# Performance work log

Measured on AMD Instinct MI355X. Metric: run time of the kernel, lower is better.

The kernel has to match this reference:

```python
import jax, jax.numpy as jnp
import numpy as np

N_ENT = 50000
N_REL = 200
DIM = 128
N_BASES = 4
NUM_RELATIONS = 2 * N_REL  # RGCNConv num_relations
E = 200000
S = 20000


def rgcn_conv(x, edge_index, edge_type, edge_norm, basis, att, root, bias, n_nodes):
    """RGCNConv with basis decomposition, aggr='mean'.
    x: [N, Din]; basis: [B, Din, Dout]; att: [R, B]; root: [Din, Dout]; bias: [Dout].
    """
    src, dst = edge_index[0], edge_index[1]
    x_j = x[src]                      # [E, Din] gather
    att_e = att[edge_type]            # [E, B]
    # message: x_j @ (att_e @ basis) without materializing per-edge [Din,Dout] weights
    msg = jnp.einsum('ei,bio,eb->eo', x_j, basis, att_e)  # [E, Dout]
    msg = msg * edge_norm[:, None]
    agg = jax.ops.segment_sum(msg, dst, num_segments=n_nodes)            # [N, Dout]
    cnt = jax.ops.segment_sum(jnp.ones_like(edge_norm), dst, num_segments=n_nodes)
    agg = agg / jnp.maximum(cnt, 1.0)[:, None]            # mean aggregation
    return agg + x @ root + bias


def setup_inputs() -> dict:
    key = jax.random.key(0)
    ks = jax.random.split(key, 20)
    d = {}
    d['entity'] = jnp.arange(N_ENT, dtype=jnp.int64) if jax.config.read('jax_enable_x64') else jnp.arange(N_ENT, dtype=jnp.int32)
    d['edge_index'] = jax.random.randint(ks[0], (2, E), 0, N_ENT)
    d['edge_type'] = jax.random.randint(ks[1], (E,), 0, NUM_RELATIONS)
    d['edge_norm'] = jax.random.uniform(ks[2], (E,), dtype=jnp.float32)
    d['samples'] = jax.random.randint(ks[3], (S, 3), 0, N_REL)
    d['DAD_rel'] = jax.random.normal(ks[4], (N_REL, N_REL), dtype=jnp.float32) * 0.05
    # learned parameters
    d['entity_emb'] = jax.random.normal(ks[5], (N_ENT, DIM), dtype=jnp.float32) * 0.02
    d['relation_emb'] = jax.random.normal(ks[6], (N_REL, DIM), dtype=jnp.float32) * 0.02
    d['entity_context_tab'] = jax.random.normal(ks[7], (N_ENT, DIM), dtype=jnp.float32) * 0.02
    d['relation_context_tab'] = jax.random.normal(ks[8], (N_REL, DIM), dtype=jnp.float32) * 0.02
    d['relation_gcn_weight'] = jax.random.normal(ks[9], (DIM, DIM), dtype=jnp.float32) * 0.02
    d['gate_entity'] = jax.random.uniform(ks[10], (DIM,), dtype=jnp.float32)
    d['gate_relation'] = jax.random.uniform(ks[11], (DIM,), dtype=jnp.float32)
    d['basis1'] = jax.random.normal(ks[12], (N_BASES, DIM, DIM), dtype=jnp.float32) * 0.02
    d['att1'] = jax.random.normal(ks[13], (NUM_RELATIONS, N_BASES), dtype=jnp.float32) * 0.1
    d['root1'] = jax.random.normal(ks[14], (DIM, DIM), dtype=jnp.float32) * 0.02
    d['bias1'] = jnp.zeros((DIM,), dtype=jnp.float32)
    d['basis2'] = jax.random.normal(ks[15], (N_BASES, DIM, DIM), dtype=jnp.float32) * 0.02
    d['att2'] = jax.random.normal(ks[16], (NUM_RELATIONS, N_BASES), dtype=jnp.float32) * 0.1
    d['root2'] = jax.random.normal(ks[17], (DIM, DIM), dtype=jnp.float32) * 0.02
    d['bias2'] = jnp.zeros((DIM,), dtype=jnp.float32)
    return d


def reference(entity, edge_index, edge_type, edge_norm, samples, DAD_rel,
              entity_emb, relation_emb, entity_context_tab, relation_context_tab,
              relation_gcn_weight, gate_entity, gate_relation,
              basis1, att1, root1, bias1, basis2, att2, root2, bias2):
    n_nodes = entity.shape[0]
    ent_ctx = entity_context_tab[entity]                  # [N, D]
    rel_ctx = relation_context_tab                        # arange over all relations -> full table
    ent_ctx = jax.nn.relu(rgcn_conv(ent_ctx, edge_index, edge_type, edge_norm,
                                    basis1, att1, root1, bias1, n_nodes))
    ent_ctx = jax.nn.relu(rgcn_conv(ent_ctx, edge_index, edge_type, edge_norm,
                                    basis2, att2, root2, bias2, n_nodes))
    rel_ctx = jax.nn.relu((DAD_rel @ rel_ctx) @ relation_gcn_weight)
    ge = jax.nn.sigmoid(gate_entity)
    gr = jax.nn.sigmoid(gate_relation)
    h, r, t = samples[:, 0], samples[:, 1], samples[:, 2]
    head_o = ge * entity_emb[h] + (1.0 - ge) * ent_ctx[h]
    rel_o = gr * relation_emb[r] + (1.0 - gr) * rel_ctx[r]
    tail_o = ge * entity_emb[t] + (1.0 - ge) * ent_ctx[t]
    return jnp.stack([head_o, rel_o, tail_o])             # [3, S, D]
```

## Files before the change

### kernel.cpp

```cpp
#include <hip/hip_runtime.h>
#include <hip/hip_bf16.h>

typedef short s8v  __attribute__((ext_vector_type(8)));
typedef float f16v __attribute__((ext_vector_type(16)));

__device__ __forceinline__ unsigned short f2bf(float x) {
    unsigned u = __float_as_uint(x);
    unsigned r = ((u >> 16) & 1u) + 0x7FFFu;
    return (unsigned short)((u + r) >> 16);
}
__device__ __forceinline__ float bf2f(unsigned short h) {
    return __uint_as_float(((unsigned)h) << 16);
}

__global__ __launch_bounds__(256) void prep_kernel(
    const float* __restrict__ basis1, const float* __restrict__ root1,
    const float* __restrict__ basis2, const float* __restrict__ root2,
    unsigned short* __restrict__ Bp1h, unsigned short* __restrict__ Bp2h,
    const int* __restrict__ edge_index, int* __restrict__ deg, int E,
    const float* __restrict__ DAD, const float* __restrict__ rtab,
    const float* __restrict__ Wrel, float* __restrict__ Rc, int NR,
    int b1, int b2)
{
    __shared__ float smem[384];
    const int b = blockIdx.x, tid = threadIdx.x;

    if (b < b1) {
        float* part = smem;
        float* r1s  = smem + 256;
        int r = b;
        int o = tid & 127, q = tid >> 7;
        float s = 0.f;
        for (int j = q; j < NR; j += 2)
            s = fmaf(DAD[r * NR + j], rtab[j * 128 + o], s);
        part[q * 128 + o] = s;
        __syncthreads();
        if (tid < 128) r1s[tid] = part[tid] + part[128 + tid];
        __syncthreads();
        float s2 = 0.f;
        #pragma unroll 8
        for (int k = q * 64; k < q * 64 + 64; ++k)
            s2 = fmaf(r1s[k], Wrel[k * 128 + o], s2);
        part[q * 128 + o] = s2;
        __syncthreads();
        if (tid < 128)
            Rc[r * 128 + tid] = fmaxf(part[tid] + part[128 + tid], 0.f);
    } else if (b < b2) {
        int bb = b - b1;
        int layer = bb >= 320;
        int idx = (layer ? bb - 320 : bb) * 256 + tid;
        int n = idx & 127, k = idx >> 7;
        const float* basis = layer ? basis2 : basis1;
        const float* root  = layer ? root2  : root1;
        float v = (k < 512) ? basis[((k & 3) << 14) + ((k >> 2) << 7) + n]
                            : root[((k - 512) << 7) + n];
        size_t pos = (((size_t)(k >> 3) * 128) + n) * 8 + (k & 7);
        (layer ? Bp2h : Bp1h)[pos] = f2bf(v);
    } else {
        int e = (b - b2) * 256 + tid;
        if (e < E) atomicAdd(&deg[edge_index[E + e]], 1);
    }
}

__global__ __launch_bounds__(1024) void scanA_kernel(
    const int* __restrict__ deg, int* __restrict__ row_start,
    int* __restrict__ btot, int N)
{
    __shared__ int wtot[16];
    __shared__ int woff[16];
    const int tid = threadIdx.x, lane = tid & 63, wid = tid >> 6;
    int i = blockIdx.x * 1024 + tid;
    int v = (i < N) ? deg[i] : 0;
    int x = v;
    #pragma unroll
    for (int d = 1; d < 64; d <<= 1) {
        int t = __shfl_up(x, d, 64);
        if (lane >= d) x += t;
    }
    if (lane == 63) wtot[wid] = x;
    __syncthreads();
    if (wid == 0 && lane < 16) {
        int s = wtot[lane];
        int y = s;
        #pragma unroll
        for (int d = 1; d < 16; d <<= 1) {
            int t = __shfl_up(y, d, 16);
            if (lane >= d) y += t;
        }
        woff[lane] = y - s;
        if (lane == 15) btot[blockIdx.x] = y;
    }
    __syncthreads();
    if (i < N) row_start[i] = woff[wid] + (x - v);
}

__global__ __launch_bounds__(1024) void scanC_kernel(
    int* __restrict__ row_start, int* __restrict__ cursor,
    const int* __restrict__ btot, int nB, int N)
{
    __shared__ int incl[64];
    const int tid = threadIdx.x;
    if (tid < 64) {
        int v = (tid < nB) ? btot[tid] : 0;
        int x = v;
        #pragma unroll
        for (int d = 1; d < 64; d <<= 1) {
            int t = __shfl_up(x, d, 64);
            if (tid >= d) x += t;
        }
        incl[tid] = x;
    }
    __syncthreads();
    int off = (blockIdx.x == 0) ? 0 : incl[blockIdx.x - 1];
    int i = blockIdx.x * 1024 + tid;
    if (i < N) {
        int r = row_start[i] + off;
        row_start[i] = r;
        cursor[i]    = r;
    }
    if (blockIdx.x == (unsigned)(nB - 1) && tid == 0)
        row_start[N] = incl[nB - 1];
}

__global__ __launch_bounds__(256) void fill_kernel(
    const int* __restrict__ edge_index, const int* __restrict__ edge_type,
    const float* __restrict__ edge_norm, int* __restrict__ cursor,
    const float* __restrict__ att1, const float* __restrict__ att2,
    int* __restrict__ src_s, float4* __restrict__ an1, float4* __restrict__ an2, int E,
    const float* __restrict__ tab, const int* __restrict__ entity,
    unsigned short* __restrict__ X0h, unsigned short* __restrict__ X0l, int N,
    int fblocks)
{
    const int b = blockIdx.x, tid = threadIdx.x;
    if (b < fblocks) {
        int e = b * 256 + tid;
        if (e >= E) return;
        int dst = edge_index[E + e];
        int et  = edge_type[e];
        float n = edge_norm[e];
        int pos = atomicAdd(&cursor[dst], 1);
        src_s[pos] = edge_index[e];
        float4 a1 = *(const float4*)&att1[(size_t)et * 4];
        float4 a2 = *(const float4*)&att2[(size_t)et * 4];
        an1[pos] = make_float4(n * a1.x, n * a1.y, n * a1.z, n * a1.w);
        an2[pos] = make_float4(n * a2.x, n * a2.y, n * a2.z, n * a2.w);
    } else {
        int idx = (b - fblocks) * 256 + tid;
        int nn = idx >> 4, part = idx & 15;
        if (nn < N) {
            int src = entity[nn];
            const float4* sp = (const float4*)&tab[(size_t)src * 128 + part * 8];
            float4 v0 = sp[0], v1 = sp[1];
            float vs[8] = {v0.x, v0.y, v0.z, v0.w, v1.x, v1.y, v1.z, v1.w};
            s8v h8, l8;
            #pragma unroll
            for (int j = 0; j < 8; ++j) {
                unsigned short h = f2bf(vs[j]);
                h8[j] = (short)h;
                l8[j] = (short)f2bf(vs[j] - bf2f(h));
            }
            *(s8v*)&X0h[(size_t)nn * 128 + part * 8] = h8;
            *(s8v*)&X0l[(size_t)nn * 128 + part * 8] = l8;
        }
    }
}

__global__ __launch_bounds__(256) void layer_kernel(
    const unsigned short* __restrict__ Xh,
    const unsigned short* __restrict__ Xl,
    const int* __restrict__ row_start,
    const int* __restrict__ src_s,
    const float4* __restrict__ an,
    const unsigned short* __restrict__ Bph,
    const float* __restrict__ bias,
    unsigned short* __restrict__ Xoh,
    unsigned short* __restrict__ Xol,
    int N)
{
    __shared__ unsigned short Whi[64 * 32 * 8];

    const int tid   = threadIdx.x;
    const int node0 = blockIdx.x * 32;

    {
        int g = tid >> 5, l = tid & 31;
        int nb = node0 + g * 4;
        int s0a[4], s1a[4];
        #pragma unroll
        for (int i = 0; i < 4; ++i) {
            int gn = nb + i;
            bool ok = gn < N;
            s0a[i] = ok ? row_start[gn] : 0;
            s1a[i] = ok ? row_start[gn + 1] : 0;
        }
        float acc[4][4][4];
        #pragma unroll
        for (int i = 0; i < 4; ++i)
            #pragma unroll
            for (int d = 0; d < 4; ++d)
                #pragma unroll
                for (int c = 0; c < 4; ++c) acc[i][d][c] = 0.f;

        int need = 0;
        #pragma unroll
        for (int i = 0; i < 4; ++i) need = max(need, s1a[i] - s0a[i]);

        for (int p = 0; p < need; p += 4) {
            #pragma unroll
            for (int i = 0; i < 4; ++i) {
                int q0 = s0a[i] + p;
                if (q0 < s1a[i]) {
                    int se = s1a[i] - 1;
                    int q1 = min(q0 + 1, se);
                    int q2 = min(q0 + 2, se);
                    int q3 = min(q0 + 3, se);
                    int sA = src_s[q0], sB = src_s[q1];
                    int sC = src_s[q2], sD = src_s[q3];
                    float4 aA = an[q0], aB = an[q1];
                    float4 aC = an[q2], aD = an[q3];
                    if (q0 + 1 > se) aB = make_float4(0.f, 0.f, 0.f, 0.f);
                    if (q0 + 2 > se) aC = make_float4(0.f, 0.f, 0.f, 0.f);
                    if (q0 + 3 > se) aD = make_float4(0.f, 0.f, 0.f, 0.f);
                    ushort4 hA = *(const ushort4*)&Xh[(size_t)sA * 128 + (l << 2)];
                    ushort4 hB = *(const ushort4*)&Xh[(size_t)sB * 128 + (l << 2)];
                    ushort4 hC = *(const ushort4*)&Xh[(size_t)sC * 128 + (l << 2)];
                    ushort4 hD = *(const ushort4*)&Xh[(size_t)sD * 128 + (l << 2)];
                    float xsA[4] = {bf2f(hA.x), bf2f(hA.y), bf2f(hA.z), bf2f(hA.w)};
                    float xsB[4] = {bf2f(hB.x), bf2f(hB.y), bf2f(hB.z), bf2f(hB.w)};
                    float xsC[4] = {bf2f(hC.x), bf2f(hC.y), bf2f(hC.z), bf2f(hC.w)};
                    float xsD[4] = {bf2f(hD.x), bf2f(hD.y), bf2f(hD.z), bf2f(hD.w)};
                    #pragma unroll
                    for (int d = 0; d < 4; ++d) {
                        acc[i][d][0] = fmaf(aA.x, xsA[d], fmaf(aB.x, xsB[d], fmaf(aC.x, xsC[d], fmaf(aD.x, xsD[d], acc[i][d][0]))));
                        acc[i][d][1] = fmaf(aA.y, xsA[d], fmaf(aB.y, xsB[d], fmaf(aC.y, xsC[d], fmaf(aD.y, xsD[d], acc[i][d][1]))));
                        acc[i][d][2] = fmaf(aA.z, xsA[d], fmaf(aB.z, xsB[d], fmaf(aC.z, xsC[d], fmaf(aD.z, xsD[d], acc[i][d][2]))));
                        acc[i][d][3] = fmaf(aA.w, xsA[d], fmaf(aB.w, xsB[d], fmaf(aC.w, xsC[d], fmaf(aD.w, xsD[d], acc[i][d][3]))));
                    }
                }
            }
        }
        #pragma unroll
        for (int i = 0; i < 4; ++i) {
            int n = g * 4 + i;
            float inv = 1.0f / fmaxf((float)(s1a[i] - s0a[i]), 1.0f);
            #pragma unroll
            for (int d = 0; d < 4; ++d) {
                int kh   = 2 * l + (d >> 1);
                int slot = n ^ (kh & 31);
                ushort4 h;
                h.x = f2bf(acc[i][d][0] * inv);
                h.y = f2bf(acc[i][d][1] * inv);
                h.z = f2bf(acc[i][d][2] * inv);
                h.w = f2bf(acc[i][d][3] * inv);
                *(ushort4*)&Whi[(kh * 32 + slot) * 8 + (d & 1) * 4] = h;
            }
        }
    }

    const int lane = tid & 63, wv = tid >> 6;
    const int m    = lane & 31;
    const int kh8  = lane >> 5;
    const s8v z8 = {0, 0, 0, 0, 0, 0, 0, 0};
    s8v xh[8], xl[8];
    {
        int gn  = node0 + m;
        bool ok = gn < N;
        size_t xbase = (size_t)(ok ? gn : 0) * 128;
        #pragma unroll
        for (int q = 0; q < 8; ++q) {
            int dk = 2 * q + kh8;
            xh[q] = *(const s8v*)&Xh[xbase + dk * 8];
            xl[q] = *(const s8v*)&Xl[xbase + dk * 8];
        }
        if (!ok) {
            #pragma unroll
            for (int q = 0; q < 8; ++q) { xh[q] = z8; xl[q] = z8; }
        }
    }
    __syncthreads();

    const int c0 = wv << 5;

    f16v acc;
    #pragma unroll
    for (int i = 0; i < 16; ++i) acc[i] = 0.f;

    s8v Bb[2][4];
    auto khg_of = [&](int t) {
        return (t < 8) ? (64 + 2 * t + kh8) : (2 * (t - 8) + kh8);
    };
    auto loadB4 = [&](int g, int buf) {
        #pragma unroll
        for (int q = 0; q < 4; ++q) {
            int khg = khg_of(g * 4 + q);
            size_t off = ((size_t)khg * 128 + c0 + m) * 8;
            Bb[buf][q] = *(const s8v*)&Bph[off];
        }
    };
    loadB4(0, 0);

    #pragma unroll
    for (int g = 0; g < 10; ++g) {
        int buf = g & 1;
        if (g < 9) loadB4(g + 1, buf ^ 1);
        #pragma unroll
        for (int q = 0; q < 4; ++q) {
            int t = g * 4 + q;
            if (t < 8) {
                acc = __builtin_amdgcn_mfma_f32_32x32x16_bf16(xl[t], Bb[buf][q], acc, 0, 0, 0);
                acc = __builtin_amdgcn_mfma_f32_32x32x16_bf16(xh[t], Bb[buf][q], acc, 0, 0, 0);
            } else {
                int khg  = 2 * (t - 8) + kh8;
                int slot = m ^ (khg & 31);
                s8v aH = *(const s8v*)&Whi[(khg * 32 + slot) * 8];
                acc = __builtin_amdgcn_mfma_f32_32x32x16_bf16(aH, Bb[buf][q], acc, 0, 0, 0);
            }
        }
    }

    int gc = c0 + m;
    float bv = bias[gc];
    const int rbase = kh8 << 2;
    #pragma unroll
    for (int reg = 0; reg < 16; ++reg) {
        int gr = node0 + rbase + (reg & 3) + ((reg >> 2) << 3);
        if (gr < N) {
            float v = fmaxf(acc[reg] + bv, 0.f);
            unsigned short h = f2bf(v);
            Xoh[(size_t)gr * 128 + gc] = h;
            Xol[(size_t)gr * 128 + gc] = f2bf(v - bf2f(h));
        }
    }
}

__global__ __launch_bounds__(256) void output_kernel(
    const int* __restrict__ samples,
    const float* __restrict__ gate_e,
    const float* __restrict__ gate_r,
    const float* __restrict__ ent_emb,
    const float* __restrict__ rel_emb,
    const unsigned short* __restrict__ ctx2h,
    const unsigned short* __restrict__ ctx2l,
    const float* __restrict__ relctx,
    float* __restrict__ out, int S)
{
    int s = blockIdx.x * 2 + (threadIdx.x >> 7);
    if (s >= S) return;
    int p = blockIdx.y;
    int o = threadIdx.x & 127;
    float v;
    if (p == 1) {
        int idx = samples[s * 3 + 1];
        float g = 1.0f / (1.0f + __expf(-gate_r[o]));
        v = g * rel_emb[idx * 128 + o] + (1.0f - g) * relctx[idx * 128 + o];
    } else {
        int idx = samples[s * 3 + (p == 0 ? 0 : 2)];
        float g = 1.0f / (1.0f + __expf(-gate_e[o]));
        float c = bf2f(ctx2h[(size_t)idx * 128 + o]) + bf2f(ctx2l[(size_t)idx * 128 + o]);
        v = g * ent_emb[(size_t)idx * 128 + o] + (1.0f - g) * c;
    }
    out[(size_t)p * S * 128 + (size_t)s * 128 + o] = v;
}

extern "C" void kernel_launch(void* const* d_in, const int* in_sizes, int n_in,
                              void* d_out, int out_size, void* d_ws, size_t ws_size,
                              hipStream_t stream)
{
    const int*   entity     = (const int*)d_in[0];
    const int*   edge_index = (const int*)d_in[1];
    const int*   edge_type  = (const int*)d_in[2];
    const float* edge_norm  = (const float*)d_in[3];
    const int*   samples    = (const int*)d_in[4];
    const float* DAD        = (const float*)d_in[5];
    const float* ent_emb    = (const float*)d_in[6];
    const float* rel_emb    = (const float*)d_in[7];
    const float* ent_tab    = (const float*)d_in[8];
    const float* rel_tab    = (const float*)d_in[9];
    const float* Wrel       = (const float*)d_in[10];
    const float* gate_e     = (const float*)d_in[11];
    const float* gate_r     = (const float*)d_in[12];
    const float* basis1     = (const float*)d_in[13];
    const float* att1       = (const float*)d_in[14];
    const float* root1      = (const float*)d_in[15];
    const float* bias1      = (const float*)d_in[16];
    const float* basis2     = (const float*)d_in[17];
    const float* att2       = (const float*)d_in[18];
    const float* root2      = (const float*)d_in[19];
    const float* bias2      = (const float*)d_in[20];

    const int N  = in_sizes[0];
    const int E  = in_sizes[2];
    const int S  = in_sizes[4] / 3;
    const int NR = in_sizes[9] / 128;

    unsigned short* X0h = (unsigned short*)d_ws;
    unsigned short* X0l = X0h + (size_t)N * 128;
    unsigned short* X1h = X0l + (size_t)N * 128;
    unsigned short* X1l = X1h + (size_t)N * 128;
    float4* an1    = (float4*)(X1l + (size_t)N * 128);
    float4* an2    = an1 + (E + 4);
    float* Rc      = (float*)(an2 + (E + 4));
    int*   deg     = (int*)(Rc + (size_t)NR * 128);
    int*   rstart  = deg + N;
    int*   cursor  = rstart + N + 1;
    int*   src_s   = cursor + N;
    int*   btot    = src_s + E + 4;
    int*   boff    = btot + 64;
    uintptr_t bt   = ((uintptr_t)(boff + 64) + 15) & ~(uintptr_t)15;
    unsigned short* Bp1h = (unsigned short*)bt;
    unsigned short* Bp2h = Bp1h + 80 * 128 * 8;

    const int egrid = (E + 255) / 256;
    const int lgrid = (N + 31) / 32;
    const int nB    = (N + 1023) / 1024;
    const int x0blocks = (N * 16 + 255) / 256;
    const int b1 = NR;
    const int b2 = NR + 640;
    const int pgrid = b2 + egrid;

    hipMemsetAsync(deg, 0, (size_t)N * sizeof(int), stream);
    prep_kernel<<<pgrid, 256, 0, stream>>>(
        basis1, root1, basis2, root2, Bp1h, Bp2h,
        edge_index, deg, E,
        DAD, rel_tab, Wrel, Rc, NR, b1, b2);
    scanA_kernel<<<nB, 1024, 0, stream>>>(deg, rstart, btot, N);
    scanC_kernel<<<nB, 1024, 0, stream>>>(rstart, cursor, btot, nB, N);
    fill_kernel<<<egrid + x0blocks, 256, 0, stream>>>(
        edge_index, edge_type, edge_norm, cursor, att1, att2, src_s, an1, an2, E,
        ent_tab, entity, X0h, X0l, N, egrid);

    layer_kernel<<<lgrid, 256, 0, stream>>>(X0h, X0l, rstart, src_s, an1,
                                            Bp1h, bias1, X1h, X1l, N);
    layer_kernel<<<lgrid, 256, 0, stream>>>(X1h, X1l, rstart, src_s, an2,
                                            Bp2h, bias2, X0h, X0l, N);

    output_kernel<<<dim3((S + 1) / 2, 3), 256, 0, stream>>>(
        samples, gate_e, gate_r, ent_emb, rel_emb, X0h, X0l, Rc, (float*)d_out, S);
}
```

Before: 307.5 us.

## Split histogram from prep, merge prep into fill, and give each node its own aggregation group

The degree histogram moves into its own kernel, and the relation-GCN, weight-packing and fill work are merged into one mega kernel launched after the scans. The layer kernel now uses 512 threads, so each 16-thread group aggregates a single node with 8-wide bf16 loads. Before, one group walked four nodes at once and looped to the largest of their degrees. After aggregation the upper half of the block exits and the lower 256 threads run the MFMA phase. The output kernel has each thread handle 4 samples and computes the gate sigmoid once per thread. The aim is to remove degree-imbalance idling and improve gather parallelism, at the cost of a larger block and more register pressure.

```diff
diff --git a/kernel.cpp b/kernel.cpp
--- a/kernel.cpp
+++ b/kernel.cpp
@@ -13,19 +13,91 @@
     return __uint_as_float(((unsigned)h) << 16);
 }
 
-__global__ __launch_bounds__(256) void prep_kernel(
+__global__ __launch_bounds__(256) void hist_kernel(
+    const int* __restrict__ edge_index, int* __restrict__ deg, int E)
+{
+    int e = blockIdx.x * 256 + threadIdx.x;
+    if (e < E) atomicAdd(&deg[edge_index[E + e]], 1);
+}
+
+__global__ __launch_bounds__(1024) void scanA_kernel(
+    const int* __restrict__ deg, int* __restrict__ row_start,
+    int* __restrict__ btot, int N)
+{
+    __shared__ int wtot[16];
+    __shared__ int woff[16];
+    const int tid = threadIdx.x, lane = tid & 63, wid = tid >> 6;
+    int i = blockIdx.x * 1024 + tid;
+    int v = (i < N) ? deg[i] : 0;
+    int x = v;
+    #pragma unroll
+    for (int d = 1; d < 64; d <<= 1) {
+        int t = __shfl_up(x, d, 64);
+        if (lane >= d) x += t;
+    }
+    if (lane == 63) wtot[wid] = x;
+    __syncthreads();
+    if (wid == 0 && lane < 16) {
+        int s = wtot[lane];
+        int y = s;
+        #pragma unroll
+        for (int d = 1; d < 16; d <<= 1) {
+            int t = __shfl_up(y, d, 16);
+            if (lane >= d) y += t;
+        }
+        woff[lane] = y - s;
+        if (lane == 15) btot[blockIdx.x] = y;
+    }
+    __syncthreads();
+    if (i < N) row_start[i] = woff[wid] + (x - v);
+}
+
+__global__ __launch_bounds__(1024) void scanC_kernel(
+    int* __restrict__ row_start, int* __restrict__ cursor,
+    const int* __restrict__ btot, int nB, int N)
+{
+    __shared__ int incl[64];
+    const int tid = threadIdx.x;
+    if (tid < 64) {
+        int v = (tid < nB) ? btot[tid] : 0;
+        int x = v;
+        #pragma unroll
+        for (int d = 1; d < 64; d <<= 1) {
+            int t = __shfl_up(x, d, 64);
+            if (tid >= d) x += t;
+        }
+        incl[tid] = x;
+    }
+    __syncthreads();
+    int off = (blockIdx.x == 0) ? 0 : incl[blockIdx.x - 1];
+    int i = blockIdx.x * 1024 + tid;
+    if (i < N) {
+        int r = row_start[i] + off;
+        row_start[i] = r;
+        cursor[i]    = r;
+    }
+    if (blockIdx.x == (unsigned)(nB - 1) && tid == 0)
+        row_start[N] = incl[nB - 1];
+}
+
+__global__ __launch_bounds__(256) void mega_kernel(
+    const float* __restrict__ DAD, const float* __restrict__ rtab,
+    const float* __restrict__ Wrel, float* __restrict__ Rc, int NR,
+    const int* __restrict__ edge_index, const int* __restrict__ edge_type,
+    const float* __restrict__ edge_norm, int* __restrict__ cursor,
+    const float* __restrict__ att1, const float* __restrict__ att2,
+    int* __restrict__ src_s, float4* __restrict__ an1, float4* __restrict__ an2, int E,
+    const float* __restrict__ tab, const int* __restrict__ entity,
+    unsigned short* __restrict__ X0h, unsigned short* __restrict__ X0l, int N,
     const float* __restrict__ basis1, const float* __restrict__ root1,
     const float* __restrict__ basis2, const float* __restrict__ root2,
     unsigned short* __restrict__ Bp1h, unsigned short* __restrict__ Bp2h,
-    const int* __restrict__ edge_index, int* __restrict__ deg, int E,
-    const float* __restrict__ DAD, const float* __restrict__ rtab,
-    const float* __restrict__ Wrel, float* __restrict__ Rc, int NR,
-    int b1, int b2)
+    int c1, int c2, int c3)
 {
     __shared__ float smem[384];
     const int b = blockIdx.x, tid = threadIdx.x;
 
-    if (b < b1) {
+    if (b < c1) {
         float* part = smem;
         float* r1s  = smem + 256;
         int r = b;
@@ -45,95 +117,8 @@
         __syncthreads();
         if (tid < 128)
             Rc[r * 128 + tid] = fmaxf(part[tid] + part[128 + tid], 0.f);
-    } else if (b < b2) {
-        int bb = b - b1;
-        int layer = bb >= 320;
-        int idx = (layer ? bb - 320 : bb) * 256 + tid;
-        int n = idx & 127, k = idx >> 7;
-        const float* basis = layer ? basis2 : basis1;
-        const float* root  = layer ? root2  : root1;
-        float v = (k < 512) ? basis[((k & 3) << 14) + ((k >> 2) << 7) + n]
-                            : root[((k - 512) << 7) + n];
-        size_t pos = (((size_t)(k >> 3) * 128) + n) * 8 + (k & 7);
-        (layer ? Bp2h : Bp1h)[pos] = f2bf(v);
-    } else {
-        int e = (b - b2) * 256 + tid;
-        if (e < E) atomicAdd(&deg[edge_index[E + e]], 1);
-    }
-}
-
-__global__ __launch_bounds__(1024) void scanA_kernel(
-    const int* __restrict__ deg, int* __restrict__ row_start,
-    int* __restrict__ btot, int N)
-{
-    __shared__ int wtot[16];
-    __shared__ int woff[16];
-    const int tid = threadIdx.x, lane = tid & 63, wid = tid >> 6;
-    int i = blockIdx.x * 1024 + tid;
-    int v = (i < N) ? deg[i] : 0;
-    int x = v;
-    #pragma unroll
-    for (int d = 1; d < 64; d <<= 1) {
-        int t = __shfl_up(x, d, 64);
-        if (lane >= d) x += t;
-    }
-    if (lane == 63) wtot[wid] = x;
-    __syncthreads();
-    if (wid == 0 && lane < 16) {
-        int s = wtot[lane];
-        int y = s;
-        #pragma unroll
-        for (int d = 1; d < 16; d <<= 1) {
-            int t = __shfl_up(y, d, 16);
-            if (lane >= d) y += t;
-        }
-        woff[lane] = y - s;
-        if (lane == 15) btot[blockIdx.x] = y;
-    }
-    __syncthreads();
-    if (i < N) row_start[i] = woff[wid] + (x - v);
-}
-
-__global__ __launch_bounds__(1024) void scanC_kernel(
-    int* __restrict__ row_start, int* __restrict__ cursor,
-    const int* __restrict__ btot, int nB, int N)
-{
-    __shared__ int incl[64];
-    const int tid = threadIdx.x;
-    if (tid < 64) {
-        int v = (tid < nB) ? btot[tid] : 0;
-        int x = v;
-        #pragma unroll
-        for (int d = 1; d < 64; d <<= 1) {
-            int t = __shfl_up(x, d, 64);
-            if (tid >= d) x += t;
-        }
-        incl[tid] = x;
-    }
-    __syncthreads();
-    int off = (blockIdx.x == 0) ? 0 : incl[blockIdx.x - 1];
-    int i = blockIdx.x * 1024 + tid;
-    if (i < N) {
-        int r = row_start[i] + off;
-        row_start[i] = r;
-        cursor[i]    = r;
-    }
-    if (blockIdx.x == (unsigned)(nB - 1) && tid == 0)
-        row_start[N] = incl[nB - 1];
-}
-
-__global__ __launch_bounds__(256) void fill_kernel(
-    const int* __restrict__ edge_index, const int* __restrict__ edge_type,
-    const float* __restrict__ edge_norm, int* __restrict__ cursor,
-    const float* __restrict__ att1, const float* __restrict__ att2,
-    int* __restrict__ src_s, float4* __restrict__ an1, float4* __restrict__ an2, int E,
-    const float* __restrict__ tab, const int* __restrict__ entity,
-    unsigned short* __restrict__ X0h, unsigned short* __restrict__ X0l, int N,
-    int fblocks)
-{
-    const int b = blockIdx.x, tid = threadIdx.x;
-    if (b < fblocks) {
-        int e = b * 256 + tid;
+    } else if (b < c2) {
+        int e = (b - c1) * 256 + tid;
         if (e >= E) return;
         int dst = edge_index[E + e];
         int et  = edge_type[e];
@@ -144,8 +129,8 @@
         float4 a2 = *(const float4*)&att2[(size_t)et * 4];
         an1[pos] = make_float4(n * a1.x, n * a1.y, n * a1.z, n * a1.w);
         an2[pos] = make_float4(n * a2.x, n * a2.y, n * a2.z, n * a2.w);
-    } else {
-        int idx = (b - fblocks) * 256 + tid;
+    } else if (b < c3) {
+        int idx = (b - c2) * 256 + tid;
         int nn = idx >> 4, part = idx & 15;
         if (nn < N) {
             int src = entity[nn];
@@ -162,10 +147,21 @@
             *(s8v*)&X0h[(size_t)nn * 128 + part * 8] = h8;
             *(s8v*)&X0l[(size_t)nn * 128 + part * 8] = l8;
         }
-    }
-}
-
-__global__ __launch_bounds__(256) void layer_kernel(
+    } else {
+        int bb = b - c3;
+        int layer = bb >= 320;
+        int idx = (layer ? bb - 320 : bb) * 256 + tid;
+        int n = idx & 127, k = idx >> 7;
+        const float* basis = layer ? basis2 : basis1;
+        const float* root  = layer ? root2  : root1;
+        float v = (k < 512) ? basis[((k & 3) << 14) + ((k >> 2) << 7) + n]
+                            : root[((k - 512) << 7) + n];
+        size_t pos = (((size_t)(k >> 3) * 128) + n) * 8 + (k & 7);
+        (layer ? Bp2h : Bp1h)[pos] = f2bf(v);
+    }
+}
+
+__global__ __launch_bounds__(512, 4) void layer_kernel(
     const unsigned short* __restrict__ Xh,
     const unsigned short* __restrict__ Xl,
     const int* __restrict__ row_start,
@@ -183,86 +179,66 @@
     const int node0 = blockIdx.x * 32;
 
     {
-        int g = tid >> 5, l = tid & 31;
-        int nb = node0 + g * 4;
-        int s0a[4], s1a[4];
-        #pragma unroll
-        for (int i = 0; i < 4; ++i) {
-            int gn = nb + i;
-            bool ok = gn < N;
-            s0a[i] = ok ? row_start[gn] : 0;
-            s1a[i] = ok ? row_start[gn + 1] : 0;
-        }
-        float acc[4][4][4];
-        #pragma unroll
-        for (int i = 0; i < 4; ++i)
+        const int g = tid >> 4, l = tid & 15;
+        const int gn = node0 + g;
+        const bool ok = gn < N;
+        int s0 = ok ? row_start[gn] : 0;
+        int s1 = ok ? row_start[gn + 1] : 0;
+        float acc[8][4];
+        #pragma unroll
+        for (int d = 0; d < 8; ++d)
             #pragma unroll
-            for (int d = 0; d < 4; ++d)
-                #pragma unroll
-                for (int c = 0; c < 4; ++c) acc[i][d][c] = 0.f;
-
-        int need = 0;
-        #pragma unroll
-        for (int i = 0; i < 4; ++i) need = max(need, s1a[i] - s0a[i]);
-
-        for (int p = 0; p < need; p += 4) {
+            for (int c = 0; c < 4; ++c) acc[d][c] = 0.f;
+
+        const int se = s1 - 1;
+        for (int q0 = s0; q0 < s1; q0 += 4) {
+            int q1 = min(q0 + 1, se);
+            int q2 = min(q0 + 2, se);
+            int q3 = min(q0 + 3, se);
+            int sA = src_s[q0], sB = src_s[q1];
+            int sC = src_s[q2], sD = src_s[q3];
+            float4 aA = an[q0], aB = an[q1];
+            float4 aC = an[q2], aD = an[q3];
+            if (q0 + 1 > se) aB = make_float4(0.f, 0.f, 0.f, 0.f);
+            if (q0 + 2 > se) aC = make_float4(0.f, 0.f, 0.f, 0.f);
+            if (q0 + 3 > se) aD = make_float4(0.f, 0.f, 0.f, 0.f);
+            s8v hA = *(const s8v*)&Xh[(size_t)sA * 128 + (l << 3)];
+            s8v hB = *(const s8v*)&Xh[(size_t)sB * 128 + (l << 3)];
+            s8v hC = *(const s8v*)&Xh[(size_t)sC * 128 + (l << 3)];
+            s8v hD = *(const s8v*)&Xh[(size_t)sD * 128 + (l << 3)];
             #pragma unroll
-            for (int i = 0; i < 4; ++i) {
-                int q0 = s0a[i] + p;
-                if (q0 < s1a[i]) {
-                    int se = s1a[i] - 1;
-                    int q1 = min(q0 + 1, se);
-                    int q2 = min(q0 + 2, se);
-                    int q3 = min(q0 + 3, se);
-                    int sA = src_s[q0], sB = src_s[q1];
-                    int sC = src_s[q2], sD = src_s[q3];
-                    float4 aA = an[q0], aB = an[q1];
-                    float4 aC = an[q2], aD = an[q3];
-                    if (q0 + 1 > se) aB = make_float4(0.f, 0.f, 0.f, 0.f);
-                    if (q0 + 2 > se) aC = make_float4(0.f, 0.f, 0.f, 0.f);
-                    if (q0 + 3 > se) aD = make_float4(0.f, 0.f, 0.f, 0.f);
-                    ushort4 hA = *(const ushort4*)&Xh[(size_t)sA * 128 + (l << 2)];
-                    ushort4 hB = *(const ushort4*)&Xh[(size_t)sB * 128 + (l << 2)];
-                    ushort4 hC = *(const ushort4*)&Xh[(size_t)sC * 128 + (l << 2)];
-                    ushort4 hD = *(const ushort4*)&Xh[(size_t)sD * 128 + (l << 2)];
-                    float xsA[4] = {bf2f(hA.x), bf2f(hA.y), bf2f(hA.z), bf2f(hA.w)};
-                    float xsB[4] = {bf2f(hB.x), bf2f(hB.y), bf2f(hB.z), bf2f(hB.w)};
-                    float xsC[4] = {bf2f(hC.x), bf2f(hC.y), bf2f(hC.z), bf2f(hC.w)};
-                    float xsD[4] = {bf2f(hD.x), bf2f(hD.y), bf2f(hD.z), bf2f(hD.w)};
-                    #pragma unroll
-                    for (int d = 0; d < 4; ++d) {
-                        acc[i][d][0] = fmaf(aA.x, xsA[d], fmaf(aB.x, xsB[d], fmaf(aC.x, xsC[d], fmaf(aD.x, xsD[d], acc[i][d][0]))));
-                        acc[i][d][1] = fmaf(aA.y, xsA[d], fmaf(aB.y, xsB[d], fmaf(aC.y, xsC[d], fmaf(aD.y, xsD[d], acc[i][d][1]))));
-                        acc[i][d][2] = fmaf(aA.z, xsA[d], fmaf(aB.z, xsB[d], fmaf(aC.z, xsC[d], fmaf(aD.z, xsD[d], acc[i][d][2]))));
-                        acc[i][d][3] = fmaf(aA.w, xsA[d], fmaf(aB.w, xsB[d], fmaf(aC.w, xsC[d], fmaf(aD.w, xsD[d], acc[i][d][3]))));
-                    }
-                }
+            for (int d = 0; d < 8; ++d) {
+                float xA = bf2f((unsigned short)hA[d]);
+                float xB = bf2f((unsigned short)hB[d]);
+                float xC = bf2f((unsigned short)hC[d]);
+                float xD = bf2f((unsigned short)hD[d]);
+                acc[d][0] = fmaf(aA.x, xA, fmaf(aB.x, xB, fmaf(aC.x, xC, fmaf(aD.x, xD, acc[d][0]))));
+                acc[d][1] = fmaf(aA.y, xA, fmaf(aB.y, xB, fmaf(aC.y, xC, fmaf(aD.y, xD, acc[d][1]))));
+                acc[d][2] = fmaf(aA.z, xA, fmaf(aB.z, xB, fmaf(aC.z, xC, fmaf(aD.z, xD, acc[d][2]))));
+                acc[d][3] = fmaf(aA.w, xA, fmaf(aB.w, xB, fmaf(aC.w, xC, fmaf(aD.w, xD, acc[d][3]))));
             }
         }
-        #pragma unroll
-        for (int i = 0; i < 4; ++i) {
-            int n = g * 4 + i;
-            float inv = 1.0f / fmaxf((float)(s1a[i] - s0a[i]), 1.0f);
+        float inv = 1.0f / fmaxf((float)(s1 - s0), 1.0f);
+        #pragma unroll
+        for (int f = 0; f < 4; ++f) {
+            int kh   = 4 * l + f;
+            int slot = g ^ (kh & 31);
+            s8v h8;
             #pragma unroll
-            for (int d = 0; d < 4; ++d) {
-                int kh   = 2 * l + (d >> 1);
-                int slot = n ^ (kh & 31);
-                ushort4 h;
-                h.x = f2bf(acc[i][d][0] * inv);
-                h.y = f2bf(acc[i][d][1] * inv);
-                h.z = f2bf(acc[i][d][2] * inv);
-                h.w = f2bf(acc[i][d][3] * inv);
-                *(ushort4*)&Whi[(kh * 32 + slot) * 8 + (d & 1) * 4] = h;
+            for (int j = 0; j < 4; ++j) {
+                h8[j]     = (short)f2bf(acc[2 * f][j]     * inv);
+                h8[4 + j] = (short)f2bf(acc[2 * f + 1][j] * inv);
             }
+            *(s8v*)&Whi[(kh * 32 + slot) * 8] = h8;
         }
     }
 
     const int lane = tid & 63, wv = tid >> 6;
     const int m    = lane & 31;
     const int kh8  = lane >> 5;
-    const s8v z8 = {0, 0, 0, 0, 0, 0, 0, 0};
     s8v xh[8], xl[8];
-    {
+    if (tid < 256) {
+        const s8v z8 = {0, 0, 0, 0, 0, 0, 0, 0};
         int gn  = node0 + m;
         bool ok = gn < N;
         size_t xbase = (size_t)(ok ? gn : 0) * 128;
@@ -278,6 +254,7 @@
         }
     }
     __syncthreads();
+    if (tid >= 256) return;
 
     const int c0 = wv << 5;
 
@@ -344,22 +321,27 @@
     const float* __restrict__ relctx,
     float* __restrict__ out, int S)
 {
-    int s = blockIdx.x * 2 + (threadIdx.x >> 7);
-    if (s >= S) return;
-    int p = blockIdx.y;
-    int o = threadIdx.x & 127;
-    float v;
-    if (p == 1) {
-        int idx = samples[s * 3 + 1];
-        float g = 1.0f / (1.0f + __expf(-gate_r[o]));
-        v = g * rel_emb[idx * 128 + o] + (1.0f - g) * relctx[idx * 128 + o];
-    } else {
-        int idx = samples[s * 3 + (p == 0 ? 0 : 2)];
-        float g = 1.0f / (1.0f + __expf(-gate_e[o]));
-        float c = bf2f(ctx2h[(size_t)idx * 128 + o]) + bf2f(ctx2l[(size_t)idx * 128 + o]);
-        v = g * ent_emb[(size_t)idx * 128 + o] + (1.0f - g) * c;
-    }
-    out[(size_t)p * S * 128 + (size_t)s * 128 + o] = v;
+    const int p   = blockIdx.y;
+    const int o   = threadIdx.x & 127;
+    const int sub = threadIdx.x >> 7;
+    const float g = (p == 1) ? 1.0f / (1.0f + __expf(-gate_r[o]))
+                             : 1.0f / (1.0f + __expf(-gate_e[o]));
+    const int s0 = blockIdx.x * 8 + sub;
+    #pragma unroll
+    for (int k = 0; k < 4; ++k) {
+        int s = s0 + k * 2;
+        if (s >= S) break;
+        float v;
+        if (p == 1) {
+            int idx = samples[s * 3 + 1];
+            v = g * rel_emb[idx * 128 + o] + (1.0f - g) * relctx[idx * 128 + o];
+        } else {
+            int idx = samples[s * 3 + (p == 0 ? 0 : 2)];
+            float c = bf2f(ctx2h[(size_t)idx * 128 + o]) + bf2f(ctx2l[(size_t)idx * 128 + o]);
+            v = g * ent_emb[(size_t)idx * 128 + o] + (1.0f - g) * c;
+        }
+        out[(size_t)p * S * 128 + (size_t)s * 128 + o] = v;
+    }
 }
 
 extern "C" void kernel_launch(void* const* d_in, const int* in_sizes, int n_in,
@@ -414,26 +396,27 @@
     const int lgrid = (N + 31) / 32;
     const int nB    = (N + 1023) / 1024;
     const int x0blocks = (N * 16 + 255) / 256;
-    const int b1 = NR;
-    const int b2 = NR + 640;
-    const int pgrid = b2 + egrid;
+    const int c1 = NR;
+    const int c2 = c1 + egrid;
+    const int c3 = c2 + x0blocks;
+    const int mgrid = c3 + 640;
 
     hipMemsetAsync(deg, 0, (size_t)N * sizeof(int), stream);
-    prep_kernel<<<pgrid, 256, 0, stream>>>(
-        basis1, root1, basis2, root2, Bp1h, Bp2h,
-        edge_index, deg, E,
-        DAD, rel_tab, Wrel, Rc, NR, b1, b2);
+    hist_kernel<<<egrid, 256, 0, stream>>>(edge_index, deg, E);
     scanA_kernel<<<nB, 1024, 0, stream>>>(deg, rstart, btot, N);
     scanC_kernel<<<nB, 1024, 0, stream>>>(rstart, cursor, btot, nB, N);
-    fill_kernel<<<egrid + x0blocks, 256, 0, stream>>>(
+    mega_kernel<<<mgrid, 256, 0, stream>>>(
+        DAD, rel_tab, Wrel, Rc, NR,
         edge_index, edge_type, edge_norm, cursor, att1, att2, src_s, an1, an2, E,
-        ent_tab, entity, X0h, X0l, N, egrid);
-
-    layer_kernel<<<lgrid, 256, 0, stream>>>(X0h, X0l, rstart, src_s, an1,
+        ent_tab, entity, X0h, X0l, N,
+        basis1, root1, basis2, root2, Bp1h, Bp2h,
+        c1, c2, c3);
+
+    layer_kernel<<<lgrid, 512, 0, stream>>>(X0h, X0l, rstart, src_s, an1,
                                             Bp1h, bias1, X1h, X1l, N);
-    layer_kernel<<<lgrid, 256, 0, stream>>>(X1h, X1l, rstart, src_s, an2,
+    layer_kernel<<<lgrid, 512, 0, stream>>>(X1h, X1l, rstart, src_s, an2,
                                             Bp2h, bias2, X0h, X0l, N);
 
-    output_kernel<<<dim3((S + 1) / 2, 3), 256, 0, stream>>>(
+    output_kernel<<<dim3((S + 7) / 8, 3), 256, 0, stream>>>(
         samples, gate_e, gate_r, ent_emb, rel_emb, X0h, X0l, Rc, (float*)d_out, S);
 }
```

Result: faster. 295.1 us (-4.0%).
